# Optimization experiments

Hardware: AMD Instinct MI355X
Metric: run time of the kernel (lower is better)

## Reference

```python
import jax, jax.numpy as jnp
import numpy as np

N_EMBD = 1024
N_HEAD = 16
HEAD_DIM = N_EMBD // N_HEAD
NEG = -1e9


def setup_inputs() -> dict:
    key = jax.random.key(0)
    ks = jax.random.split(key, 5)
    B, S = 2, 2048
    x = jax.random.normal(ks[0], (B, S, N_EMBD), dtype=jnp.float32)
    # qkv_proj: Linear(n_embd, 3*n_embd) -> weight used as x @ W_qkv (W stored [in, out])
    scale = 1.0 / np.sqrt(N_EMBD)
    W_qkv = jax.random.normal(ks[1], (N_EMBD, 3 * N_EMBD), dtype=jnp.float32) * scale
    b_qkv = jax.random.normal(ks[2], (3 * N_EMBD,), dtype=jnp.float32) * 0.02
    W_out = jax.random.normal(ks[3], (N_EMBD, N_EMBD), dtype=jnp.float32) * scale
    b_out = jax.random.normal(ks[4], (N_EMBD,), dtype=jnp.float32) * 0.02
    return {"x": x, "W_qkv": W_qkv, "b_qkv": b_qkv, "W_out": W_out, "b_out": b_out}


def reference(x, W_qkv, b_qkv, W_out, b_out):
    B, S, E = x.shape
    qkv = x @ W_qkv + b_qkv                      # [B,S,3E]
    q, k, v = jnp.split(qkv, 3, axis=-1)
    # [B,S,E] -> [B,H,S,D]
    def split_heads(t):
        return t.reshape(B, S, N_HEAD, HEAD_DIM).transpose(0, 2, 1, 3)
    q, k, v = split_heads(q), split_heads(k), split_heads(v)
    scores = jnp.einsum("bhqd,bhkd->bhqk", q, k) / jnp.sqrt(jnp.float32(HEAD_DIM))
    causal = jnp.tril(jnp.ones((S, S), dtype=bool))
    scores = jnp.where(causal, scores, NEG)
    attn = jax.nn.softmax(scores, axis=-1)
    out = jnp.einsum("bhqk,bhkd->bhqd", attn, v)  # [B,H,S,D]
    out = out.transpose(0, 2, 1, 3).reshape(B, S, E)
    return out @ W_out + b_out
```

## Files before the change

### kernel.cpp

```cpp
#include <hip/hip_runtime.h>
#include <hip/hip_bf16.h>

#define BATCH 2
#define SEQ   2048
#define EMBD  1024
#define NHEAD 16
#define HDIM  64
#define QKV3  (3 * EMBD)

typedef __attribute__((ext_vector_type(8))) __bf16 bf16x8;
typedef __attribute__((ext_vector_type(4))) __bf16 bf16x4;
typedef __attribute__((ext_vector_type(4))) float f32x4;

__global__ __launch_bounds__(256) void cast_f32_bf16(
    const float* __restrict__ in, __bf16* __restrict__ out)
{
    int i = (blockIdx.x * 256 + threadIdx.x) * 8;
    float4 a = *(const float4*)&in[i];
    float4 b = *(const float4*)&in[i + 4];
    bf16x8 o;
    o[0] = (__bf16)a.x; o[1] = (__bf16)a.y; o[2] = (__bf16)a.z; o[3] = (__bf16)a.w;
    o[4] = (__bf16)b.x; o[5] = (__bf16)b.y; o[6] = (__bf16)b.z; o[7] = (__bf16)b.w;
    *(bf16x8*)&out[i] = o;
}

__global__ __launch_bounds__(256) void transpose_cast_bf16(
    const float* __restrict__ in, __bf16* __restrict__ out, int K, int N)
{
    __shared__ float t[64][65];
    const int k0 = blockIdx.y * 64, n0 = blockIdx.x * 64;
    const int tid = threadIdx.x;
    #pragma unroll
    for (int p = 0; p < 4; p++) {
        int kr = p * 16 + (tid >> 4);
        int c4 = (tid & 15) * 4;
        float4 v = *(const float4*)&in[(size_t)(k0 + kr) * N + n0 + c4];
        t[kr][c4] = v.x; t[kr][c4 + 1] = v.y; t[kr][c4 + 2] = v.z; t[kr][c4 + 3] = v.w;
    }
    __syncthreads();
    #pragma unroll
    for (int p = 0; p < 4; p++) {
        int nr = p * 16 + (tid >> 4);
        int k4 = (tid & 15) * 4;
        bf16x4 o;
        o[0] = (__bf16)t[k4 + 0][nr];
        o[1] = (__bf16)t[k4 + 1][nr];
        o[2] = (__bf16)t[k4 + 2][nr];
        o[3] = (__bf16)t[k4 + 3][nr];
        *(bf16x4*)&out[(size_t)(n0 + nr) * K + k0 + k4] = o;
    }
}

__global__ __launch_bounds__(256) void transpose_v_bf16(
    const __bf16* __restrict__ qkv, __bf16* __restrict__ vt)
{
    __shared__ __bf16 t[64][72];
    const int k0 = blockIdx.x * 64;
    const int bh = blockIdx.y;
    const int b = bh >> 4, h = bh & 15;
    const size_t base = (size_t)b * SEQ * QKV3 + 2 * EMBD + h * HDIM;
    const int tid = threadIdx.x;
    #pragma unroll
    for (int it = 0; it < 2; it++) {
        int flat = it * 256 + tid;
        int kr = flat >> 3;
        int d0 = (flat & 7) * 8;
        bf16x8 v = *(const bf16x8*)&qkv[base + (size_t)(k0 + kr) * QKV3 + d0];
        #pragma unroll
        for (int i = 0; i < 8; i++) t[kr][d0 + i] = v[i];
    }
    __syncthreads();
    #pragma unroll
    for (int it = 0; it < 2; it++) {
        int flat = it * 256 + tid;
        int d  = flat >> 3;
        int kc = (flat & 7) * 8;
        bf16x8 o;
        #pragma unroll
        for (int i = 0; i < 8; i++) o[i] = t[kc + i][d];
        *(bf16x8*)&vt[((size_t)bh * 64 + d) * SEQ + k0 + kc] = o;
    }
}

template<bool OUT_BF16>
__global__ __launch_bounds__(256) void gemm_bt_mfma(
    const __bf16* __restrict__ A,
    const __bf16* __restrict__ Bt,
    const float* __restrict__ bias,
    void* __restrict__ Cv,
    int M, int N, int K, int nscale)
{
    __shared__ __align__(16) __bf16 As[128 * 32];
    __shared__ __align__(16) __bf16 Bs[128 * 32];

    const int tid  = threadIdx.x;
    const int lane = tid & 63;
    const int wave = tid >> 6;
    const int wm = (wave >> 1) * 64;
    const int wn = (wave & 1) * 64;
    const int m0 = blockIdx.y * 128;
    const int n0 = blockIdx.x * 128;
    const int lm = lane & 15;
    const int kq = lane >> 4;

    f32x4 acc[4][4] = {};

    for (int k0 = 0; k0 < K; k0 += 32) {
        __syncthreads();
        #pragma unroll
        for (int r = 0; r < 2; r++) {
            int flat = r * 256 + tid;
            int row  = flat >> 2;
            int off  = (flat & 3) * 16;
            const char* ga = (const char*)(A + (size_t)(m0 + row) * K + k0) + off;
            char* la = (char*)As + flat * 16;
            __builtin_amdgcn_global_load_lds(
                (const __attribute__((address_space(1))) void*)ga,
                (__attribute__((address_space(3))) void*)la, 16, 0, 0);
            const char* gb = (const char*)(Bt + (size_t)(n0 + row) * K + k0) + off;
            char* lb = (char*)Bs + flat * 16;
            __builtin_amdgcn_global_load_lds(
                (const __attribute__((address_space(1))) void*)gb,
                (__attribute__((address_space(3))) void*)lb, 16, 0, 0);
        }
        __syncthreads();

        bf16x8 af[4], bf[4];
        #pragma unroll
        for (int t = 0; t < 4; t++) {
            af[t] = *(const bf16x8*)&As[(wm + t * 16 + lm) * 32 + kq * 8];
            bf[t] = *(const bf16x8*)&Bs[(wn + t * 16 + lm) * 32 + kq * 8];
        }
        #pragma unroll
        for (int i = 0; i < 4; i++)
            #pragma unroll
            for (int j = 0; j < 4; j++)
                acc[i][j] = __builtin_amdgcn_mfma_f32_16x16x32_bf16(
                    af[i], bf[j], acc[i][j], 0, 0, 0);
    }

    const int r0 = kq * 4;
    #pragma unroll
    for (int i = 0; i < 4; i++) {
        #pragma unroll
        for (int j = 0; j < 4; j++) {
            int col = n0 + wn + j * 16 + lm;
            float bv = bias[col];
            float sc = (col < nscale) ? 0.125f : 1.0f;
            #pragma unroll
            for (int r = 0; r < 4; r++) {
                int row = m0 + wm + i * 16 + r0 + r;
                float val = (acc[i][j][r] + bv) * sc;
                if (OUT_BF16) ((__bf16*)Cv)[(size_t)row * N + col] = (__bf16)val;
                else          ((float*)Cv)[(size_t)row * N + col] = val;
            }
        }
    }
}

__global__ __launch_bounds__(256) void attn_kpar_mfma(
    const __bf16* __restrict__ qkv, const __bf16* __restrict__ vt,
    __bf16* __restrict__ attn)
{
    __shared__ __align__(16) char smem[16896];

    const int tid  = threadIdx.x;
    const int wave = tid >> 6;
    const int lane = tid & 63;
    const int quad = lane >> 4;
    const int c    = lane & 15;

    const int bh = blockIdx.x;
    const int b  = bh >> 4;
    const int h  = bh & 15;
    const int qblk = (int)(gridDim.y - 1) - blockIdx.y;
    const int q0 = qblk * 32;

    const size_t base = (size_t)b * SEQ * QKV3;
    const int hoff = h * HDIM;
    const __bf16* vbase = vt + (size_t)bh * 64 * SEQ;

    bf16x8 aq[2][2];
    #pragma unroll
    for (int qf = 0; qf < 2; qf++) {
        const __bf16* qrow = qkv + base +
            (size_t)(q0 + qf * 16 + c) * QKV3 + hoff + quad * 8;
        aq[qf][0] = *(const bf16x8*)(qrow);
        aq[qf][1] = *(const bf16x8*)(qrow + 32);
    }

    f32x4 acc[2][4] = {};
    float lpart[2][4] = {};

    char* pbw = smem + wave * 4096;
    const int ntiles = q0 / 64 + 1;

    for (int t = wave; t < ntiles; t += 4) {
        const int k0 = t * 64;
        const bool diag = (t == ntiles - 1);

        #pragma unroll
        for (int jj = 0; jj < 4; jj++) {
            const __bf16* krow = qkv + base +
                (size_t)(k0 + jj * 16 + c) * QKV3 + EMBD + hoff + quad * 8;
            bf16x8 bk0 = *(const bf16x8*)(krow);
            bf16x8 bk1 = *(const bf16x8*)(krow + 32);
            const int kabs_c = k0 + jj * 16 + c;
            const int col = jj * 16 + c;
            const int ab = (col >> 5) * 1024 + ((col >> 3) & 3) * 256 + (col & 7) * 2;
            #pragma unroll
            for (int qf = 0; qf < 2; qf++) {
                f32x4 s = {};
                s = __builtin_amdgcn_mfma_f32_16x16x32_bf16(aq[qf][0], bk0, s, 0, 0, 0);
                s = __builtin_amdgcn_mfma_f32_16x16x32_bf16(aq[qf][1], bk1, s, 0, 0, 0);
                char* pq = pbw + qf * 2048 + ab;
                const int qabs0 = q0 + qf * 16 + quad * 4;
                #pragma unroll
                for (int r = 0; r < 4; r++) {
                    float p;
                    if (diag && (kabs_c > qabs0 + r)) p = 0.f;
                    else p = __expf(fminf(s[r], 60.f));
                    lpart[qf][r] += p;
                    *(__bf16*)(pq + (quad * 4 + r) * 16) = (__bf16)p;
                }
            }
        }

        bf16x8 ap[2][2];
        #pragma unroll
        for (int qf = 0; qf < 2; qf++) {
            ap[qf][0] = *(const bf16x8*)(pbw + qf * 2048 + lane * 16);
            ap[qf][1] = *(const bf16x8*)(pbw + qf * 2048 + 1024 + lane * 16);
        }

        #pragma unroll
        for (int dd = 0; dd < 4; dd++) {
            const __bf16* vr = vbase + (size_t)(dd * 16 + c) * SEQ + k0 + quad * 8;
            bf16x8 bv0 = *(const bf16x8*)(vr);
            bf16x8 bv1 = *(const bf16x8*)(vr + 32);
            #pragma unroll
            for (int qf = 0; qf < 2; qf++) {
                acc[qf][dd] = __builtin_amdgcn_mfma_f32_16x16x32_bf16(ap[qf][0], bv0, acc[qf][dd], 0, 0, 0);
                acc[qf][dd] = __builtin_amdgcn_mfma_f32_16x16x32_bf16(ap[qf][1], bv1, acc[qf][dd], 0, 0, 0);
            }
        }
    }

    #pragma unroll
    for (int qf = 0; qf < 2; qf++)
        #pragma unroll
        for (int r = 0; r < 4; r++) {
            float v = lpart[qf][r];
            v += __shfl_xor(v, 1);
            v += __shfl_xor(v, 2);
            v += __shfl_xor(v, 4);
            v += __shfl_xor(v, 8);
            lpart[qf][r] = v;
        }

    __syncthreads();

    float* Ored = (float*)smem;
    float* lred = (float*)(smem + 16640);

    if (wave < 2) {
        float* R = Ored + wave * (32 * 65);
        #pragma unroll
        for (int qf = 0; qf < 2; qf++)
            #pragma unroll
            for (int dd = 0; dd < 4; dd++)
                #pragma unroll
                for (int r = 0; r < 4; r++)
                    R[(qf * 16 + quad * 4 + r) * 65 + dd * 16 + c] = acc[qf][dd][r];
        if (c == 0) {
            #pragma unroll
            for (int qf = 0; qf < 2; qf++)
                #pragma unroll
                for (int r = 0; r < 4; r++)
                    lred[wave * 32 + qf * 16 + quad * 4 + r] = lpart[qf][r];
        }
    }
    __syncthreads();
    if (wave >= 2) {
        float* R = Ored + (wave - 2) * (32 * 65);
        #pragma unroll
        for (int qf = 0; qf < 2; qf++)
            #pragma unroll
            for (int dd = 0; dd < 4; dd++)
                #pragma unroll
                for (int r = 0; r < 4; r++)
                    R[(qf * 16 + quad * 4 + r) * 65 + dd * 16 + c] += acc[qf][dd][r];
        if (c == 0) {
            #pragma unroll
            for (int qf = 0; qf < 2; qf++)
                #pragma unroll
                for (int r = 0; r < 4; r++)
                    lred[(wave - 2) * 32 + qf * 16 + quad * 4 + r] += lpart[qf][r];
        }
    }
    __syncthreads();

    {
        const int row = tid >> 3;
        const int cg  = tid & 7;
        const float l = lred[row] + lred[32 + row];
        const float inv = 1.f / l;
        const float* R0 = Ored + row * 65 + cg * 8;
        const float* R1 = R0 + 32 * 65;
        bf16x8 o;
        #pragma unroll
        for (int i = 0; i < 8; i++) o[i] = (__bf16)((R0[i] + R1[i]) * inv);
        *(bf16x8*)&attn[((size_t)b * SEQ + q0 + row) * EMBD + hoff + cg * 8] = o;
    }
}

extern "C" void kernel_launch(void* const* d_in, const int* in_sizes, int n_in,
                              void* d_out, int out_size, void* d_ws, size_t ws_size,
                              hipStream_t stream)
{
    const float* x     = (const float*)d_in[0];
    const float* W_qkv = (const float*)d_in[1];
    const float* b_qkv = (const float*)d_in[2];
    const float* W_out = (const float*)d_in[3];
    const float* b_out = (const float*)d_in[4];
    float* out = (float*)d_out;

    const int M = BATCH * SEQ;

    __bf16* xbf    = (__bf16*)d_ws;
    __bf16* Wqkv_t = xbf    + (size_t)M * EMBD;
    __bf16* Wout_t = Wqkv_t + (size_t)QKV3 * EMBD;
    __bf16* qkv    = Wout_t + (size_t)EMBD * EMBD;
    __bf16* attn   = qkv    + (size_t)M * QKV3;
    __bf16* vtbuf  = attn   + (size_t)M * EMBD;

    cast_f32_bf16<<<(M * EMBD) / (256 * 8), 256, 0, stream>>>(x, xbf);
    {
        dim3 g(QKV3 / 64, EMBD / 64);
        transpose_cast_bf16<<<g, 256, 0, stream>>>(W_qkv, Wqkv_t, EMBD, QKV3);
    }
    {
        dim3 g(EMBD / 64, EMBD / 64);
        transpose_cast_bf16<<<g, 256, 0, stream>>>(W_out, Wout_t, EMBD, EMBD);
    }
    {
        dim3 grid(QKV3 / 128, M / 128);
        gemm_bt_mfma<true><<<grid, 256, 0, stream>>>(xbf, Wqkv_t, b_qkv, qkv, M, QKV3, EMBD, EMBD);
    }
    {
        dim3 grid(SEQ / 64, BATCH * NHEAD);
        transpose_v_bf16<<<grid, 256, 0, stream>>>(qkv, vtbuf);
    }
    {
        dim3 grid(BATCH * NHEAD, SEQ / 32);
        attn_kpar_mfma<<<grid, 256, 0, stream>>>(qkv, vtbuf, attn);
    }
    {
        dim3 grid(EMBD / 128, M / 128);
        gemm_bt_mfma<false><<<grid, 256, 0, stream>>>(attn, Wout_t, b_out, out, M, EMBD, EMBD, 0);
    }
}
```

Measured before the change: 219.6 us.

## Prefetch K and V tiles into registers and use exp2 with folded log2e scale

```diff
diff --git a/kernel.cpp b/kernel.cpp
--- a/kernel.cpp
+++ b/kernel.cpp
@@ -11,6 +11,8 @@
 typedef __attribute__((ext_vector_type(8))) __bf16 bf16x8;
 typedef __attribute__((ext_vector_type(4))) __bf16 bf16x4;
 typedef __attribute__((ext_vector_type(4))) float f32x4;
+
+#define QSCALE 0.18033688011112043f
 
 __global__ __launch_bounds__(256) void cast_f32_bf16(
     const float* __restrict__ in, __bf16* __restrict__ out)
@@ -146,7 +148,7 @@
         for (int j = 0; j < 4; j++) {
             int col = n0 + wn + j * 16 + lm;
             float bv = bias[col];
-            float sc = (col < nscale) ? 0.125f : 1.0f;
+            float sc = (col < nscale) ? QSCALE : 1.0f;
             #pragma unroll
             for (int r = 0; r < 4; r++) {
                 int row = m0 + wm + i * 16 + r0 + r;
@@ -158,7 +160,7 @@
     }
 }
 
-__global__ __launch_bounds__(256) void attn_kpar_mfma(
+__global__ __launch_bounds__(256, 3) void attn_kpar_mfma(
     const __bf16* __restrict__ qkv, const __bf16* __restrict__ vt,
     __bf16* __restrict__ attn)
 {
@@ -195,31 +197,67 @@
     char* pbw = smem + wave * 4096;
     const int ntiles = q0 / 64 + 1;
 
+    bf16x8 bk[4][2];
+    if (wave < ntiles) {
+        const int k0 = wave * 64;
+        #pragma unroll
+        for (int jj = 0; jj < 4; jj++) {
+            const __bf16* krow = qkv + base +
+                (size_t)(k0 + jj * 16 + c) * QKV3 + EMBD + hoff + quad * 8;
+            bk[jj][0] = *(const bf16x8*)(krow);
+            bk[jj][1] = *(const bf16x8*)(krow + 32);
+        }
+    }
+
     for (int t = wave; t < ntiles; t += 4) {
         const int k0 = t * 64;
         const bool diag = (t == ntiles - 1);
 
+        bf16x8 bv[4][2];
+        #pragma unroll
+        for (int dd = 0; dd < 4; dd++) {
+            const __bf16* vr = vbase + (size_t)(dd * 16 + c) * SEQ + k0 + quad * 8;
+            bv[dd][0] = *(const bf16x8*)(vr);
+            bv[dd][1] = *(const bf16x8*)(vr + 32);
+        }
+
+        f32x4 S[2][4];
         #pragma unroll
         for (int jj = 0; jj < 4; jj++) {
-            const __bf16* krow = qkv + base +
-                (size_t)(k0 + jj * 16 + c) * QKV3 + EMBD + hoff + quad * 8;
-            bf16x8 bk0 = *(const bf16x8*)(krow);
-            bf16x8 bk1 = *(const bf16x8*)(krow + 32);
-            const int kabs_c = k0 + jj * 16 + c;
-            const int col = jj * 16 + c;
-            const int ab = (col >> 5) * 1024 + ((col >> 3) & 3) * 256 + (col & 7) * 2;
             #pragma unroll
             for (int qf = 0; qf < 2; qf++) {
                 f32x4 s = {};
-                s = __builtin_amdgcn_mfma_f32_16x16x32_bf16(aq[qf][0], bk0, s, 0, 0, 0);
-                s = __builtin_amdgcn_mfma_f32_16x16x32_bf16(aq[qf][1], bk1, s, 0, 0, 0);
+                s = __builtin_amdgcn_mfma_f32_16x16x32_bf16(aq[qf][0], bk[jj][0], s, 0, 0, 0);
+                s = __builtin_amdgcn_mfma_f32_16x16x32_bf16(aq[qf][1], bk[jj][1], s, 0, 0, 0);
+                S[qf][jj] = s;
+            }
+        }
+
+        if (t + 4 < ntiles) {
+            const int kn = k0 + 256;
+            #pragma unroll
+            for (int jj = 0; jj < 4; jj++) {
+                const __bf16* krow = qkv + base +
+                    (size_t)(kn + jj * 16 + c) * QKV3 + EMBD + hoff + quad * 8;
+                bk[jj][0] = *(const bf16x8*)(krow);
+                bk[jj][1] = *(const bf16x8*)(krow + 32);
+            }
+        }
+
+        #pragma unroll
+        for (int jj = 0; jj < 4; jj++) {
+            const int col = jj * 16 + c;
+            const int kabs_c = k0 + col;
+            const int ab = (col >> 5) * 1024 + ((col >> 3) & 3) * 256 + (col & 7) * 2;
+            #pragma unroll
+            for (int qf = 0; qf < 2; qf++) {
                 char* pq = pbw + qf * 2048 + ab;
                 const int qabs0 = q0 + qf * 16 + quad * 4;
                 #pragma unroll
                 for (int r = 0; r < 4; r++) {
                     float p;
                     if (diag && (kabs_c > qabs0 + r)) p = 0.f;
-                    else p = __expf(fminf(s[r], 60.f));
+                    else p = __builtin_amdgcn_exp2f(S[qf][jj][r]);
                     lpart[qf][r] += p;
                     *(__bf16*)(pq + (quad * 4 + r) * 16) = (__bf16)p;
                 }
@@ -235,13 +273,10 @@
 
         #pragma unroll
         for (int dd = 0; dd < 4; dd++) {
-            const __bf16* vr = vbase + (size_t)(dd * 16 + c) * SEQ + k0 + quad * 8;
-            bf16x8 bv0 = *(const bf16x8*)(vr);
-            bf16x8 bv1 = *(const bf16x8*)(vr + 32);
             #pragma unroll
             for (int qf = 0; qf < 2; qf++) {
-                acc[qf][dd] = __builtin_amdgcn_mfma_f32_16x16x32_bf16(ap[qf][0], bv0, acc[qf][dd], 0, 0, 0);
-                acc[qf][dd] = __builtin_amdgcn_mfma_f32_16x16x32_bf16(ap[qf][1], bv1, acc[qf][dd], 0, 0, 0);
+                acc[qf][dd] = __builtin_amdgcn_mfma_f32_16x16x32_bf16(ap[qf][0], bv[dd][0], acc[qf][dd], 0, 0, 0);
+                acc[qf][dd] = __builtin_amdgcn_mfma_f32_16x16x32_bf16(ap[qf][1], bv[dd][1], acc[qf][dd], 0, 0, 0);
             }
         }
     }
```

Measured after the change: 250.7 us. 14.2% more time.
